# Performance work log

Hardware: AMD Instinct MI355X
Metric: run time of the kernel (lower is better)

The kernel has to match this reference:

```python
import jax, jax.numpy as jnp
import numpy as np


def setup_inputs() -> dict:
    key = jax.random.key(0)
    ks = jax.random.split(key, 7)
    B, Din, H = 65536, 256, 512
    s_in = 1.0 / np.sqrt(Din)
    s_h = 1.0 / np.sqrt(H)
    return {
        "input_x": jax.random.normal(ks[0], (B, Din), jnp.float32),
        "h_old": jax.random.normal(ks[1], (B, H), jnp.float32),
        "c_old": jax.random.normal(ks[2], (B, H), jnp.float32),
        # stacked gate weights, order [i, f, o, c]
        "U": jax.random.normal(ks[3], (4, Din, H), jnp.float32) * s_in,
        "bU": jnp.zeros((4, H), jnp.float32),
        "W": jax.random.normal(ks[4], (4, H, H), jnp.float32) * s_h,
        "bW": jnp.zeros((4, H), jnp.float32),
    }


def reference(input_x, h_old, c_old, U, bU, W, bW):
    # Two fused GEMMs over all four gates: [B, 4, H]
    gx = jnp.einsum('bd,gdh->bgh', input_x, U) + bU[None, :, :]
    gh = jnp.einsum('bh,ghk->bgk', h_old, W) + bW[None, :, :]
    g = gx + gh  # [B, 4, H], gate order i, f, o, c
    i_t = jax.nn.sigmoid(g[:, 0])
    f_t = jax.nn.sigmoid(g[:, 1])
    o_t = jax.nn.sigmoid(g[:, 2])
    c_t = jnp.tanh(g[:, 3])
    c_new = i_t * c_t + f_t * c_old
    h_new = o_t * jnp.tanh(c_new)
    return (h_new, c_new)
```

## Files before the change

kernel.cpp:

```cpp
#include <hip/hip_runtime.h>
#include <stdint.h>
#include <stddef.h>

#define BATCH 65536
#define DIN   256
#define HDIM  512
#define KDIM  768
#define NDIM  2048
#define HN_ELEMS (BATCH * HDIM)

using f32x4 = __attribute__((ext_vector_type(4))) float;
using s16x8 = __attribute__((ext_vector_type(8))) short;
using u16x8 = __attribute__((ext_vector_type(8))) unsigned short;
using u32x4 = __attribute__((ext_vector_type(4))) unsigned int;

__device__ __forceinline__ unsigned short f2bf(float f) {
    union { float f; unsigned u; } v; v.f = f;
    unsigned r = v.u + 0x7fffu + ((v.u >> 16) & 1u);
    return (unsigned short)(r >> 16);
}

__device__ __forceinline__ unsigned pk2(float lo, float hi) {
    unsigned r;
    asm("v_cvt_pk_bf16_f32 %0, %1, %2" : "=v"(r) : "v"(lo), "v"(hi));
    return r;
}

__global__ __launch_bounds__(256) void pack_w_kernel(
    const float* __restrict__ U, const float* __restrict__ W,
    unsigned short* __restrict__ wPack)
{
    int idx = blockIdx.x * 256 + threadIdx.x;
    int n = idx / 96;
    int seg = idx - n * 96;
    int k0 = seg * 8;
    int g = (n >> 4) & 3;
    int h = ((n >> 6) << 4) | (n & 15);
    u16x8 o;
    if (k0 < DIN) {
        const float* src = U + ((size_t)g * DIN + k0) * HDIM + h;
#pragma unroll
        for (int kk = 0; kk < 8; ++kk) o[kk] = f2bf(src[(size_t)kk * HDIM]);
    } else {
        const float* src = W + ((size_t)g * HDIM + (k0 - DIN)) * HDIM + h;
#pragma unroll
        for (int kk = 0; kk < 8; ++kk) o[kk] = f2bf(src[(size_t)kk * HDIM]);
    }
    *(u16x8*)(wPack + (size_t)n * KDIM + k0) = o;
}

__global__ __launch_bounds__(256) void pack_bias_kernel(
    const float* __restrict__ bU, const float* __restrict__ bW,
    float* __restrict__ bias)
{
    int n = blockIdx.x * 256 + threadIdx.x;
    int g = (n >> 4) & 3;
    int h = ((n >> 6) << 4) | (n & 15);
    bias[n] = bU[g * HDIM + h] + bW[g * HDIM + h];
}

__global__ __launch_bounds__(256, 3) void lstm_fused_kernel(
    const float* __restrict__ x,
    const float* __restrict__ hOld,
    const unsigned short* __restrict__ wPack,
    const float* __restrict__ bias,
    const float* __restrict__ cOld,
    float* __restrict__ out)
{
    __shared__ __align__(16) unsigned short smem[16384];

    const int tid = threadIdx.x;
    const int w  = tid >> 6;
    const int l  = tid & 63;
    const int wm = w >> 1;
    const int wn = w & 1;
    const int lq = l >> 4;
    const int lc = l & 15;

    const int bid = blockIdx.x;
    const int wg  = (bid & 7) * 1024 + (bid >> 3);
    const int nt  = wg & 15;
    const int mt  = wg >> 4;
    const int m0  = mt * 128;
    const int n0  = nt * 128;

    const int ar = tid >> 1;
    const int ah = tid & 1;
    const float* xrow = x    + (size_t)(m0 + ar) * DIN  + ah * 16;
    const float* hrow = hOld + (size_t)(m0 + ar) * HDIM + ah * 16;
    const int akey = (ar >> 2) & 3;
    const int as0 = ((ah * 2)     ^ akey) * 8;
    const int as1 = ((ah * 2 + 1) ^ akey) * 8;

    const int brow_l = l >> 2;
    const int bchunk = (l & 3) ^ ((l >> 4) & 3);
    const unsigned short* gb0 = wPack + (size_t)(n0 + w * 16 + brow_l) * KDIM + bchunk * 8;
    const unsigned short* gb1 = gb0 + (size_t)64 * KDIM;

    const int swz = (lc >> 2) & 3;

    f32x4 acc[4][4];
#pragma unroll
    for (int i = 0; i < 4; ++i)
#pragma unroll
        for (int j = 0; j < 4; ++j)
            acc[i][j] = (f32x4){0.f, 0.f, 0.f, 0.f};

    {
        f32x4 av0 = ((const f32x4*)xrow)[0];
        f32x4 av1 = ((const f32x4*)xrow)[1];
        f32x4 av2 = ((const f32x4*)xrow)[2];
        f32x4 av3 = ((const f32x4*)xrow)[3];
        __builtin_amdgcn_global_load_lds(
            (const __attribute__((address_space(1))) void*)gb0,
            (__attribute__((address_space(3))) void*)&smem[8192 + w * 512], 16, 0, 0);
        __builtin_amdgcn_global_load_lds(
            (const __attribute__((address_space(1))) void*)gb1,
            (__attribute__((address_space(3))) void*)&smem[8192 + 2048 + w * 512], 16, 0, 0);
        u32x4 o0, o1;
        o0[0] = pk2(av0[0], av0[1]); o0[1] = pk2(av0[2], av0[3]);
        o0[2] = pk2(av1[0], av1[1]); o0[3] = pk2(av1[2], av1[3]);
        o1[0] = pk2(av2[0], av2[1]); o1[1] = pk2(av2[2], av2[3]);
        o1[2] = pk2(av3[0], av3[1]); o1[3] = pk2(av3[2], av3[3]);
        *(u32x4*)&smem[ar * 32 + as0] = o0;
        *(u32x4*)&smem[ar * 32 + as1] = o1;
    }
    __syncthreads();

    auto step = [&](int kt, int cur) {
        const int nxt = cur ^ 1;
        f32x4 av0, av1, av2, av3;
        const bool pf = (kt < 23);
        if (pf) {
            const int k2 = kt + 1;
            const float* s = (k2 < 8) ? (xrow + k2 * 32) : (hrow + (k2 - 8) * 32);
            av0 = ((const f32x4*)s)[0];
            av1 = ((const f32x4*)s)[1];
            av2 = ((const f32x4*)s)[2];
            av3 = ((const f32x4*)s)[3];
            const int bb = 8192 + nxt * 4096;
            __builtin_amdgcn_global_load_lds(
                (const __attribute__((address_space(1))) void*)(gb0 + k2 * 32),
                (__attribute__((address_space(3))) void*)&smem[bb + w * 512], 16, 0, 0);
            __builtin_amdgcn_global_load_lds(
                (const __attribute__((address_space(1))) void*)(gb1 + k2 * 32),
                (__attribute__((address_space(3))) void*)&smem[bb + 2048 + w * 512], 16, 0, 0);
        }
        {
            const int ab = cur * 4096;
            const int bb = 8192 + cur * 4096;
            s16x8 af[4], bf4[4];
#pragma unroll
            for (int i = 0; i < 4; ++i)
                af[i] = *(const s16x8*)&smem[ab + (wm * 64 + i * 16 + lc) * 32 + (lq ^ swz) * 8];
#pragma unroll
            for (int j = 0; j < 4; ++j)
                bf4[j] = *(const s16x8*)&smem[bb + (wn * 64 + j * 16 + lc) * 32 + (lq ^ swz) * 8];
#pragma unroll
            for (int i = 0; i < 4; ++i)
#pragma unroll
                for (int j = 0; j < 4; ++j)
                    acc[i][j] = __builtin_amdgcn_mfma_f32_16x16x32_bf16(
                        af[i], bf4[j], acc[i][j], 0, 0, 0);
        }
        if (pf) {
            u32x4 o0, o1;
            o0[0] = pk2(av0[0], av0[1]); o0[1] = pk2(av0[2], av0[3]);
            o0[2] = pk2(av1[0], av1[1]); o0[3] = pk2(av1[2], av1[3]);
            o1[0] = pk2(av2[0], av2[1]); o1[1] = pk2(av2[2], av2[3]);
            o1[2] = pk2(av3[0], av3[1]); o1[3] = pk2(av3[2], av3[3]);
            *(u32x4*)&smem[nxt * 4096 + ar * 32 + as0] = o0;
            *(u32x4*)&smem[nxt * 4096 + ar * 32 + as1] = o1;
        }
        __syncthreads();
    };
#pragma unroll 1
    for (int kt = 0; kt < 24; kt += 2) {
        step(kt, 0);
        step(kt + 1, 1);
    }

    const int nbase = n0 + wn * 64;
    const float b0 = bias[nbase +  0 + lc];
    const float b1 = bias[nbase + 16 + lc];
    const float b2 = bias[nbase + 32 + lc];
    const float b3 = bias[nbase + 48 + lc];
    const int hcol = (n0 >> 2) + wn * 16 + lc;

    float co[4][4];
#pragma unroll
    for (int i = 0; i < 4; ++i)
#pragma unroll
        for (int r = 0; r < 4; ++r)
            co[i][r] = cOld[(size_t)(m0 + wm * 64 + i * 16 + lq * 4 + r) * HDIM + hcol];

    float* fsm  = (float*)smem;
    float* hn_t = fsm;
    float* cn_t = fsm + 1152;

#pragma unroll
    for (int i = 0; i < 4; ++i) {
        f32x4 hnv, cnv;
#pragma unroll
        for (int r = 0; r < 4; ++r) {
            const float gi = acc[i][0][r] + b0;
            const float gf = acc[i][1][r] + b1;
            const float go = acc[i][2][r] + b2;
            const float gc = acc[i][3][r] + b3;
            const float it = 1.f / (1.f + __expf(-gi));
            const float ft = 1.f / (1.f + __expf(-gf));
            const float ot = 1.f / (1.f + __expf(-go));
            const float ct = 2.f / (1.f + __expf(-2.f * gc)) - 1.f;
            const float cn = it * ct + ft * co[i][r];
            const float tc = 2.f / (1.f + __expf(-2.f * cn)) - 1.f;
            cnv[r] = cn;
            hnv[r] = ot * tc;
        }
        __syncthreads();
        {
            const int addr = (wn * 16 + lc) * 36 + wm * 16 + lq * 4;
            *(f32x4*)&hn_t[addr] = hnv;
            *(f32x4*)&cn_t[addr] = cnv;
        }
        __syncthreads();
        {
            const int rloc = tid >> 3;
            const int cg   = tid & 7;
            const int grow = m0 + (rloc >> 4) * 64 + i * 16 + (rloc & 15);
            f32x4 hv, cv;
#pragma unroll
            for (int c = 0; c < 4; ++c) {
                hv[c] = hn_t[(cg * 4 + c) * 36 + rloc];
                cv[c] = cn_t[(cg * 4 + c) * 36 + rloc];
            }
            const size_t ob = (size_t)grow * HDIM + (n0 >> 2) + cg * 4;
            *(f32x4*)&out[ob] = hv;
            *(f32x4*)&out[(size_t)HN_ELEMS + ob] = cv;
        }
    }
}

extern "C" void kernel_launch(void* const* d_in, const int* in_sizes, int n_in,
                              void* d_out, int out_size, void* d_ws, size_t ws_size,
                              hipStream_t stream)
{
    const float* x     = (const float*)d_in[0];
    const float* h_old = (const float*)d_in[1];
    const float* c_old = (const float*)d_in[2];
    const float* U     = (const float*)d_in[3];
    const float* bU    = (const float*)d_in[4];
    const float* W     = (const float*)d_in[5];
    const float* bW    = (const float*)d_in[6];
    float* out = (float*)d_out;

    unsigned short* wPack = (unsigned short*)d_ws;
    float* bias = (float*)((char*)d_ws + (size_t)NDIM * KDIM * 2);

    pack_w_kernel<<<dim3(768), dim3(256), 0, stream>>>(U, W, wPack);
    pack_bias_kernel<<<dim3(8), dim3(256), 0, stream>>>(bU, bW, bias);
    lstm_fused_kernel<<<dim3(8192), dim3(256), 0, stream>>>(x, h_old, wPack, bias, c_old, out);
}
```

Baseline: 769.8 us.

## Triple-buffer weight tiles with two-ahead prefetch and rewrite pack kernel transpose

```diff
diff --git a/kernel.cpp b/kernel.cpp
--- a/kernel.cpp
+++ b/kernel.cpp
@@ -26,27 +26,45 @@
     return r;
 }
 
+#define GLDS(gptr, lptr) __builtin_amdgcn_global_load_lds( \
+    (const __attribute__((address_space(1))) void*)(gptr), \
+    (__attribute__((address_space(3))) void*)(lptr), 16, 0, 0)
+
 __global__ __launch_bounds__(256) void pack_w_kernel(
     const float* __restrict__ U, const float* __restrict__ W,
     unsigned short* __restrict__ wPack)
 {
-    int idx = blockIdx.x * 256 + threadIdx.x;
-    int n = idx / 96;
-    int seg = idx - n * 96;
-    int k0 = seg * 8;
-    int g = (n >> 4) & 3;
-    int h = ((n >> 6) << 4) | (n & 15);
-    u16x8 o;
-    if (k0 < DIN) {
-        const float* src = U + ((size_t)g * DIN + k0) * HDIM + h;
-#pragma unroll
-        for (int kk = 0; kk < 8; ++kk) o[kk] = f2bf(src[(size_t)kk * HDIM]);
-    } else {
-        const float* src = W + ((size_t)g * HDIM + (k0 - DIN)) * HDIM + h;
-#pragma unroll
-        for (int kk = 0; kk < 8; ++kk) o[kk] = f2bf(src[(size_t)kk * HDIM]);
-    }
-    *(u16x8*)(wPack + (size_t)n * KDIM + k0) = o;
+    __shared__ __align__(16) unsigned short lt[64 * 72];
+    const int t  = threadIdx.x;
+    const int b  = blockIdx.x;
+    const int g  = b & 3;
+    const int ht = (b >> 2) & 7;
+    const int kt = b >> 5;
+    const int k0 = kt * 64;
+    const int h0 = ht * 64;
+    const int c0 = (t & 15) * 4;
+    const int r0 = t >> 4;
+
+    const float* src = (k0 < DIN)
+        ? (U + (size_t)(g * DIN + k0 + r0) * HDIM + h0 + c0)
+        : (W + (size_t)(g * HDIM + (k0 - DIN) + r0) * HDIM + h0 + c0);
+#pragma unroll
+    for (int rr = 0; rr < 4; ++rr) {
+        f32x4 v = *(const f32x4*)(src + (size_t)rr * 16 * HDIM);
+        const int r = r0 + rr * 16;
+#pragma unroll
+        for (int j = 0; j < 4; ++j)
+            lt[(c0 + j) * 72 + r] = f2bf(v[j]);
+    }
+    __syncthreads();
+#pragma unroll
+    for (int it = 0; it < 2; ++it) {
+        const int hl = (t >> 3) + it * 32;
+        const int ks = t & 7;
+        const int n  = (ht * 4 + (hl >> 4)) * 64 + g * 16 + (hl & 15);
+        *(u16x8*)(wPack + (size_t)n * KDIM + k0 + ks * 8) =
+            *(const u16x8*)&lt[hl * 72 + ks * 8];
+    }
 }
 
 __global__ __launch_bounds__(256) void pack_bias_kernel(
@@ -67,7 +85,7 @@
     const float* __restrict__ cOld,
     float* __restrict__ out)
 {
-    __shared__ __align__(16) unsigned short smem[16384];
+    __shared__ __align__(16) unsigned short smem[20480];
 
     const int tid = threadIdx.x;
     const int w  = tid >> 6;
@@ -111,12 +129,10 @@
         f32x4 av1 = ((const f32x4*)xrow)[1];
         f32x4 av2 = ((const f32x4*)xrow)[2];
         f32x4 av3 = ((const f32x4*)xrow)[3];
-        __builtin_amdgcn_global_load_lds(
-            (const __attribute__((address_space(1))) void*)gb0,
-            (__attribute__((address_space(3))) void*)&smem[8192 + w * 512], 16, 0, 0);
-        __builtin_amdgcn_global_load_lds(
-            (const __attribute__((address_space(1))) void*)gb1,
-            (__attribute__((address_space(3))) void*)&smem[8192 + 2048 + w * 512], 16, 0, 0);
+        GLDS(gb0,      &smem[8192 + w * 512]);
+        GLDS(gb1,      &smem[8192 + 2048 + w * 512]);
+        GLDS(gb0 + 32, &smem[8192 + 4096 + w * 512]);
+        GLDS(gb1 + 32, &smem[8192 + 4096 + 2048 + w * 512]);
         u32x4 o0, o1;
         o0[0] = pk2(av0[0], av0[1]); o0[1] = pk2(av0[2], av0[3]);
         o0[2] = pk2(av1[0], av1[1]); o0[3] = pk2(av1[2], av1[3]);
@@ -124,61 +140,84 @@
         o1[2] = pk2(av3[0], av3[1]); o1[3] = pk2(av3[2], av3[3]);
         *(u32x4*)&smem[ar * 32 + as0] = o0;
         *(u32x4*)&smem[ar * 32 + as1] = o1;
-    }
-    __syncthreads();
-
-    auto step = [&](int kt, int cur) {
-        const int nxt = cur ^ 1;
+        asm volatile("s_waitcnt vmcnt(2) lgkmcnt(0)" ::: "memory");
+        __builtin_amdgcn_s_barrier();
+        __builtin_amdgcn_sched_barrier(0);
+    }
+
+    auto step = [&](int kt, bool pfa, bool pfb, int ab, int bb, int nb, int wmode) {
         f32x4 av0, av1, av2, av3;
-        const bool pf = (kt < 23);
-        if (pf) {
+        if (pfa) {
             const int k2 = kt + 1;
             const float* s = (k2 < 8) ? (xrow + k2 * 32) : (hrow + (k2 - 8) * 32);
             av0 = ((const f32x4*)s)[0];
             av1 = ((const f32x4*)s)[1];
             av2 = ((const f32x4*)s)[2];
             av3 = ((const f32x4*)s)[3];
-            const int bb = 8192 + nxt * 4096;
-            __builtin_amdgcn_global_load_lds(
-                (const __attribute__((address_space(1))) void*)(gb0 + k2 * 32),
-                (__attribute__((address_space(3))) void*)&smem[bb + w * 512], 16, 0, 0);
-            __builtin_amdgcn_global_load_lds(
-                (const __attribute__((address_space(1))) void*)(gb1 + k2 * 32),
-                (__attribute__((address_space(3))) void*)&smem[bb + 2048 + w * 512], 16, 0, 0);
+        }
+        if (pfb) {
+            const int k3 = (kt + 2) * 32;
+            unsigned short* lb = &smem[8192 + nb * 4096];
+            GLDS(gb0 + k3, lb + w * 512);
+            GLDS(gb1 + k3, lb + 2048 + w * 512);
         }
         {
-            const int ab = cur * 4096;
-            const int bb = 8192 + cur * 4096;
+            const int abase = ab * 4096;
+            const int bbase = 8192 + bb * 4096;
             s16x8 af[4], bf4[4];
 #pragma unroll
             for (int i = 0; i < 4; ++i)
-                af[i] = *(const s16x8*)&smem[ab + (wm * 64 + i * 16 + lc) * 32 + (lq ^ swz) * 8];
+                af[i] = *(const s16x8*)&smem[abase + (wm * 64 + i * 16 + lc) * 32 + (lq ^ swz) * 8];
 #pragma unroll
             for (int j = 0; j < 4; ++j)
-                bf4[j] = *(const s16x8*)&smem[bb + (wn * 64 + j * 16 + lc) * 32 + (lq ^ swz) * 8];
+                bf4[j] = *(const s16x8*)&smem[bbase + (wn * 64 + j * 16 + lc) * 32 + (lq ^ swz) * 8];
+            __builtin_amdgcn_s_setprio(1);
 #pragma unroll
             for (int i = 0; i < 4; ++i)
 #pragma unroll
                 for (int j = 0; j < 4; ++j)
                     acc[i][j] = __builtin_amdgcn_mfma_f32_16x16x32_bf16(
                         af[i], bf4[j], acc[i][j], 0, 0, 0);
-        }
-        if (pf) {
+            __builtin_amdgcn_s_setprio(0);
+        }
+        if (pfa) {
             u32x4 o0, o1;
             o0[0] = pk2(av0[0], av0[1]); o0[1] = pk2(av0[2], av0[3]);
             o0[2] = pk2(av1[0], av1[1]); o0[3] = pk2(av1[2], av1[3]);
             o1[0] = pk2(av2[0], av2[1]); o1[1] = pk2(av2[2], av2[3]);
             o1[2] = pk2(av3[0], av3[1]); o1[3] = pk2(av3[2], av3[3]);
-            *(u32x4*)&smem[nxt * 4096 + ar * 32 + as0] = o0;
-            *(u32x4*)&smem[nxt * 4096 + ar * 32 + as1] = o1;
-        }
-        __syncthreads();
+            const int abn = (ab ^ 1) * 4096;
+            *(u32x4*)&smem[abn + ar * 32 + as0] = o0;
+            *(u32x4*)&smem[abn + ar * 32 + as1] = o1;
+        }
+        if (wmode == 0) {
+            asm volatile("s_waitcnt vmcnt(2) lgkmcnt(0)" ::: "memory");
+            __builtin_amdgcn_s_barrier();
+            __builtin_amdgcn_sched_barrier(0);
+        } else if (wmode == 1) {
+            asm volatile("s_waitcnt vmcnt(0) lgkmcnt(0)" ::: "memory");
+            __builtin_amdgcn_s_barrier();
+            __builtin_amdgcn_sched_barrier(0);
+        } else {
+            __syncthreads();
+        }
     };
+
 #pragma unroll 1
-    for (int kt = 0; kt < 24; kt += 2) {
-        step(kt, 0);
-        step(kt + 1, 1);
-    }
+    for (int kb = 0; kb < 18; kb += 6) {
+        step(kb + 0, true, true, 0, 0, 2, 0);
+        step(kb + 1, true, true, 1, 1, 0, 0);
+        step(kb + 2, true, true, 0, 2, 1, 0);
+        step(kb + 3, true, true, 1, 0, 2, 0);
+        step(kb + 4, true, true, 0, 1, 0, 0);
+        step(kb + 5, true, true, 1, 2, 1, 0);
+    }
+    step(18, true,  true,  0, 0, 2, 0);
+    step(19, true,  true,  1, 1, 0, 0);
+    step(20, true,  true,  0, 2, 1, 0);
+    step(21, true,  true,  1, 0, 2, 0);
+    step(22, true,  false, 0, 1, 0, 1);
+    step(23, false, false, 1, 2, 0, 2);
 
     const int nbase = n0 + wn * 64;
     const float b0 = bias[nbase +  0 + lc];
@@ -256,7 +295,7 @@
     unsigned short* wPack = (unsigned short*)d_ws;
     float* bias = (float*)((char*)d_ws + (size_t)NDIM * KDIM * 2);
 
-    pack_w_kernel<<<dim3(768), dim3(256), 0, stream>>>(U, W, wPack);
+    pack_w_kernel<<<dim3(384), dim3(256), 0, stream>>>(U, W, wPack);
     pack_bias_kernel<<<dim3(8), dim3(256), 0, stream>>>(bU, bW, bias);
     lstm_fused_kernel<<<dim3(8192), dim3(256), 0, stream>>>(x, h_old, wPack, bias, c_old, out);
 }
```

After: 794.8 us. +3.2%, slower.
